# Performance work log

Measured on AMD Instinct MI355X. Metric: run time of the kernel, lower is better.

## Reference

```python
import jax, jax.numpy as jnp
import numpy as np

LOOP = 30  # kernel last-dim / loop count from original module

def setup_inputs() -> dict:
    key = jax.random.key(0)
    kB, k1, k2 = jax.random.split(key, 3)
    B = jax.random.normal(kB, (16, 64, 32, 32), dtype=jnp.float32)
    # torch.rand -> uniform [0,1)
    kernel1 = jax.random.uniform(k1, (64, 32, 32, LOOP), dtype=jnp.float32)
    kernel2 = jax.random.uniform(k2, (64, 32, 32, LOOP), dtype=jnp.float32)
    return {"B": B, "kernel1": kernel1, "kernel2": kernel2}

def reference(B, kernel1, kernel2):
    # fftshift over the 3 spatial dims, then the 30-iteration loop is batched:
    # move loop dim to front -> (30,64,32,32), broadcast against B (batch,64,32,32).
    Bs = jnp.fft.fftshift(B, axes=(-3, -2, -1))            # (batch,64,32,32)
    k1 = jnp.moveaxis(kernel1, -1, 0)                      # (30,64,32,32)
    k2 = jnp.moveaxis(kernel2, -1, 0)
    f1 = jnp.fft.fftn(Bs[:, None] * k1, axes=(-3, -2, -1))  # (batch,30,64,32,32) complex
    f2 = jnp.fft.fftn(Bs[:, None] * k2, axes=(-3, -2, -1))
    # complex multiply-accumulate over the loop dim
    return jnp.sum(f1 * f2, axis=1)                        # (batch,64,32,32) complex
```

## Files before the change

kernel.cpp:

```cpp
#include <hip/hip_runtime.h>
#include <hip/hip_fp16.h>
#include <cstdint>
#include <cstddef>


__host__ __device__ constexpr float twc(int k) {
  switch (k & 31) {
    case 0: return 1.0f;        case 1: return 0.98078528f;
    case 2: return 0.92387953f; case 3: return 0.83146961f;
    case 4: return 0.70710678f; case 5: return 0.55557023f;
    case 6: return 0.38268343f; case 7: return 0.19509032f;
    case 8: return 0.0f;        case 9: return -0.19509032f;
    case 10: return -0.38268343f; case 11: return -0.55557023f;
    case 12: return -0.70710678f; case 13: return -0.83146961f;
    case 14: return -0.92387953f; case 15: return -0.98078528f;
    default: return 0.0f;
  }
}
__host__ __device__ constexpr float tws(int k) {
  switch (k & 31) {
    case 0: return 0.0f;        case 1: return 0.19509032f;
    case 2: return 0.38268343f; case 3: return 0.55557023f;
    case 4: return 0.70710678f; case 5: return 0.83146961f;
    case 6: return 0.92387953f; case 7: return 0.98078528f;
    case 8: return 1.0f;        case 9: return 0.98078528f;
    case 10: return 0.92387953f; case 11: return 0.83146961f;
    case 12: return 0.70710678f; case 13: return 0.55557023f;
    case 14: return 0.38268343f; case 15: return 0.19509032f;
    default: return 0.0f;
  }
}

constexpr int brN(int x, int bits) {
  int r = 0;
  for (int b = 0; b < bits; ++b) { r = (r << 1) | (x & 1); x >>= 1; }
  return r;
}

template <int N>
__device__ __forceinline__ void fftN(float* xr, float* xi) {
#pragma unroll
  for (int len = 2; len <= N; len <<= 1) {
    const int half = len >> 1;
    const int step = 32 / len;
#pragma unroll
    for (int g = 0; g < N; g += len) {
#pragma unroll
      for (int j = 0; j < half; ++j) {
        const float c = twc(j * step), s = tws(j * step);
        const int lo = g + j, hi = g + j + half;
        float vr = xr[hi] * c + xi[hi] * s;
        float vi = xi[hi] * c - xr[hi] * s;
        float ur = xr[lo], ui = xi[lo];
        xr[lo] = ur + vr; xi[lo] = ui + vi;
        xr[hi] = ur - vr; xi[hi] = ui - vi;
      }
    }
  }
}

__global__ __launch_bounds__(256) void kzero(float4* __restrict__ o, int n4) {
  int i = blockIdx.x * 256 + threadIdx.x;
  if (i < n4) o[i] = make_float4(0.f, 0.f, 0.f, 0.f);
}


__global__ __launch_bounds__(256) void kpack(const float* __restrict__ k1,
                                             const float* __restrict__ k2,
                                             float2* __restrict__ kc) {
  int d0 = blockIdx.x >> 5, d1 = blockIdx.x & 31;
  __shared__ float2 s[960];
  int base = (d0 * 32 + d1) * 960;
  for (int u = threadIdx.x; u < 960; u += 256)
    s[u] = make_float2(k1[base + u], k2[base + u]);
  __syncthreads();
  for (int w = threadIdx.x; w < 960; w += 256) {
    int i = w >> 5, d2 = w & 31;
    kc[((size_t)(i * 64 + d0) * 32 + d1) * 32 + d2] = s[d2 * 30 + i];
  }
}

__global__ __launch_bounds__(256) void kfft2d_ws(const float* __restrict__ B,
                                                 const float2* __restrict__ kc,
                                                 __half2* __restrict__ Z,
                                                 int j0) {
  __shared__ float Lr[4][32 * 33];
  __shared__ float Li[4][32 * 33];

  const int t = threadIdx.x;
  const int v = blockIdx.x >> 4;
  const int q4 = blockIdx.x & 15;
  const int job = j0 + v;
  const int b = job / 30;
  const int i = job - b * 30;

  const int g = t >> 6;
  const int bc = t & 31;
  const int hh = (t >> 5) & 1;
  const int fs = t >> 5;
  const int fr = t & 31;

  const float* Bb = B + ((size_t)b << 16);

  {
    const int n0 = (q4 << 2) | g;
    const int sn0 = (n0 + 32) & 63;
    const float* bp = Bb + (sn0 << 10);
    const int sc = (bc + 16) & 31;
    const float2* kcl = kc + (((size_t)i << 6 | n0) << 10);
#pragma unroll
    for (int vv = 0; vv < 16; ++vv) {
      const int n1 = (hh << 4) | vv;
      float bv = bp[(((n1 + 16) & 31) << 5) | sc];
      float2 kv = kcl[(n1 << 5) | bc];
      Lr[g][n1 * 33 + bc] = bv * kv.x;
      Li[g][n1 * 33 + bc] = bv * kv.y;
    }
  }
  __syncthreads();

  if (t < 128) {
    float xr[32], xi[32];
#pragma unroll
    for (int u = 0; u < 32; ++u) {
      int p = fr * 33 + brN(u, 5);
      xr[u] = Lr[fs][p]; xi[u] = Li[fs][p];
    }
    fftN<32>(xr, xi);
#pragma unroll
    for (int u = 0; u < 32; ++u) {
      int p = fr * 33 + u;
      Lr[fs][p] = xr[u]; Li[fs][p] = xi[u];
    }
  }
  __syncthreads();

  if (t < 128) {
    float xr[32], xi[32];
#pragma unroll
    for (int u = 0; u < 32; ++u) {
      int p = brN(u, 5) * 33 + fr;
      xr[u] = Lr[fs][p]; xi[u] = Li[fs][p];
    }
    fftN<32>(xr, xi);
#pragma unroll
    for (int u = 0; u < 32; ++u) {
      int p = u * 33 + fr;
      Lr[fs][p] = xr[u]; Li[fs][p] = xi[u];
    }
  }
  __syncthreads();

#pragma unroll
  for (int j = 0; j < 16; ++j) {
    int w = (j << 8) | t;
    int g2 = w >> 10, row = (w >> 5) & 31, col = w & 31;
    int d0w = (q4 << 2) | g2;
    Z[((size_t)(v * 32 + row) << 6 | d0w) << 5 | col] = __float22half2_rn(
        make_float2(Lr[g2][row * 33 + col], Li[g2][row * 33 + col]));
  }
}

__global__ __launch_bounds__(256) void kacc64(const __half2* __restrict__ Z,
                                              float* __restrict__ tmp,
                                              int b0, int cb) {
  __shared__ float Ar[64 * 33], Ai[64 * 33];
  __shared__ float Br[64 * 33], Bi[64 * 33];
  __shared__ float W64c[64], W64s[64];

  const int t = threadIdx.x;
  const int d1 = blockIdx.x & 31;
  const int r = blockIdx.x >> 5;
  const int bl = r % cb;
  const int ig = r / cb;
  const int b = b0 + bl;
  const int i0g = ig * 8;
  const int i1g = (i0g + 8) < 30 ? (i0g + 8) : 30;

  if (t < 64) {
    float sv, cv;
    __sincosf(6.283185307179586f / 64.0f * (float)t, &sv, &cv);
    W64c[t] = cv; W64s[t] = sv;
  }
  __syncthreads();

  const int qc = t >> 5;
  const int d2 = t & 31;

  float acc[8];
#pragma unroll
  for (int a = 0; a < 8; ++a) acc[a] = 0.f;

  for (int i = i0g; i < i1g; ++i) {
    const int v = bl * 30 + i;
    const __half2* zp = Z + ((size_t)(v * 32 + d1) << 11);
#pragma unroll
    for (int j = 0; j < 8; ++j) {
      int f = (j << 8) | t;
      float2 w = __half22float2(zp[f]);
      Ar[(f >> 5) * 33 + (f & 31)] = w.x;
      Ai[(f >> 5) * 33 + (f & 31)] = w.y;
    }
    __syncthreads();

    {
      float xr[8], xi[8];
#pragma unroll
      for (int u = 0; u < 8; ++u) {
        int n0 = qc + (brN(u, 3) << 3);
        xr[u] = Ar[n0 * 33 + d2]; xi[u] = Ai[n0 * 33 + d2];
      }
      fftN<8>(xr, xi);
#pragma unroll
      for (int c = 0; c < 8; ++c) {
        int m = (qc * c) & 63;
        float wc = W64c[m], ws = W64s[m];
        float hr = xr[c] * wc + xi[c] * ws;
        float hi = xi[c] * wc - xr[c] * ws;
        int q2 = (c << 3) | qc;
        Br[q2 * 33 + d2] = hr; Bi[q2 * 33 + d2] = hi;
      }
    }
    __syncthreads();

    {
      float xr[8], xi[8];
#pragma unroll
      for (int u = 0; u < 8; ++u) {
        int q2 = (qc << 3) | brN(u, 3);
        xr[u] = Br[q2 * 33 + d2]; xi[u] = Bi[q2 * 33 + d2];
      }
      fftN<8>(xr, xi);
#pragma unroll
      for (int a = 0; a < 8; ++a)
        acc[a] += 2.0f * xr[a] * xi[a];
    }
    __syncthreads();
  }

#pragma unroll
  for (int a = 0; a < 8; ++a) {
    int d0f = qc + (a << 3);
    size_t off = ((size_t)(b << 6 | d0f) << 10) | (d1 << 5) | d2;
    atomicAdd(&tmp[off], 0.25f * acc[a]);
  }
}

__global__ __launch_bounds__(256) void ksym(const float* __restrict__ tmp,
                                            float* __restrict__ out,
                                            int out_size) {
  int idx = blockIdx.x * 256 + threadIdx.x;
  if (idx >= out_size || idx >= 16 * 65536) return;
  int d2 = idx & 31, d1 = (idx >> 5) & 31, d0 = (idx >> 10) & 63, b = idx >> 16;
  int n = (b << 16) | (((64 - d0) & 63) << 10) | (((32 - d1) & 31) << 5) |
          ((32 - d2) & 31);
  out[idx] = tmp[idx] + tmp[n];
}

__global__ __launch_bounds__(256) void kfused(const float* __restrict__ B,
                                              const float* __restrict__ k1,
                                              const float* __restrict__ k2,
                                              float* __restrict__ out,
                                              int out_size) {
  __shared__ float Lr[4][32 * 33];
  __shared__ float Li[4][32 * 33];
  __shared__ float W64c[64], W64s[64];

  const int t = threadIdx.x;
  const int bid = blockIdx.x;
  const int b = bid & 15;
  const int iq = (bid >> 4) & 3;
  const int ns = bid >> 6;
  const int i0 = iq * 8;
  const int ni = (iq == 3) ? 6 : 8;
  const int k0base = ns * 8;

  if (t < 64) {
    float sv, cv;
    __sincosf(6.283185307179586f / 64.0f * (float)t, &sv, &cv);
    W64c[t] = cv; W64s[t] = sv;
  }
  __syncthreads();

  const int g = t >> 6;
  const int bc = t & 31;
  const int hh = (t >> 5) & 1;
  const int fs = t >> 5;
  const int fr = t & 31;
  const int w1 = t >> 5;
  const int w2 = t & 31;

  const float* Bb = B + ((size_t)b << 16);

  float Sig[8][4];
#pragma unroll
  for (int kg = 0; kg < 8; ++kg)
#pragma unroll
    for (int q = 0; q < 4; ++q) Sig[kg][q] = 0.f;

  for (int ii = 0; ii < ni; ++ii) {
    const int i = i0 + ii;

    float Zr[8][4], Zi[8][4];
#pragma unroll
    for (int kg = 0; kg < 8; ++kg)
#pragma unroll
      for (int q = 0; q < 4; ++q) { Zr[kg][q] = 0.f; Zi[kg][q] = 0.f; }

    for (int it = 0; it < 16; ++it) {
      const int n0 = (it << 2) | g;
      {
        const int sn0 = (n0 + 32) & 63;
        const float* bp = Bb + (sn0 << 10);
        const int sc = (bc + 16) & 31;
#pragma unroll
        for (int v = 0; v < 16; ++v) {
          const int n1 = (hh << 4) | v;
          float bv = bp[(((n1 + 16) & 31) << 5) | sc];
          int ke = (((n0 << 10) | (n1 << 5) | bc) * 30) + i;
          Lr[g][n1 * 33 + bc] = bv * k1[ke];
          Li[g][n1 * 33 + bc] = bv * k2[ke];
        }
      }
      __syncthreads();

      if (t < 128) {
        float xr[32], xi[32];
#pragma unroll
        for (int u = 0; u < 32; ++u) {
          int p = fr * 33 + brN(u, 5);
          xr[u] = Lr[fs][p]; xi[u] = Li[fs][p];
        }
        fftN<32>(xr, xi);
#pragma unroll
        for (int u = 0; u < 32; ++u) {
          int p = fr * 33 + u;
          Lr[fs][p] = xr[u]; Li[fs][p] = xi[u];
        }
      }
      __syncthreads();

      if (t < 128) {
        float xr[32], xi[32];
#pragma unroll
        for (int u = 0; u < 32; ++u) {
          int p = brN(u, 5) * 33 + fr;
          xr[u] = Lr[fs][p]; xi[u] = Li[fs][p];
        }
        fftN<32>(xr, xi);
#pragma unroll
        for (int u = 0; u < 32; ++u) {
          int p = u * 33 + fr;
          Lr[fs][p] = xr[u]; Li[fs][p] = xi[u];
        }
      }
      __syncthreads();

#pragma unroll 1
      for (int s = 0; s < 4; ++s) {
        const int n0s = (it << 2) | s;
        const int dm = n0s & 63;
        float yr[4], yi[4];
#pragma unroll
        for (int q = 0; q < 4; ++q) {
          int p = (w1 + (q << 3)) * 33 + w2;
          yr[q] = Lr[s][p]; yi[q] = Li[s][p];
        }
        int m = (k0base * n0s) & 63;
#pragma unroll
        for (int kg = 0; kg < 8; ++kg) {
          float c = W64c[m], sn = W64s[m];
#pragma unroll
          for (int q = 0; q < 4; ++q) {
            Zr[kg][q] += yr[q] * c + yi[q] * sn;
            Zi[kg][q] += yi[q] * c - yr[q] * sn;
          }
          m = (m + dm) & 63;
        }
      }
      __syncthreads();
    }

#pragma unroll
    for (int kg = 0; kg < 8; ++kg)
#pragma unroll
      for (int q = 0; q < 4; ++q)
        Sig[kg][q] += 2.0f * Zr[kg][q] * Zi[kg][q];
  }

#pragma unroll
  for (int kg = 0; kg < 8; ++kg) {
    const int k0 = k0base + kg;
    const int nk0 = (64 - k0) & 63;
#pragma unroll
    for (int q = 0; q < 4; ++q) {
      const int r1 = w1 + (q << 3);
      const float v = Sig[kg][q] * 0.25f;
      const int nr1 = (32 - r1) & 31;
      const int nw2 = (32 - w2) & 31;
      int off = (((b << 6) | k0) << 10) | (r1 << 5) | w2;
      int noff = (((b << 6) | nk0) << 10) | (nr1 << 5) | nw2;
      if (off < out_size) atomicAdd(&out[off], v);
      if (noff < out_size) atomicAdd(&out[noff], v);
    }
  }
}

extern "C" void kernel_launch(void* const* d_in, const int* in_sizes, int n_in,
                              void* d_out, int out_size, void* d_ws,
                              size_t ws_size, hipStream_t stream) {
  const float* B = (const float*)d_in[0];
  const float* k1 = (const float*)d_in[1];
  const float* k2 = (const float*)d_in[2];
  (void)in_sizes; (void)n_in;

  const size_t tmpB = 4ull << 20;
  const size_t Z1 = 30ull * 65536 * 4;
  const size_t kcB = 30ull * 65536 * 8;

  int nbcap = 0;
  if (ws_size >= tmpB + kcB + Z1)
    nbcap = (int)((ws_size - tmpB - kcB) / Z1);

  if (nbcap >= 1) {
    char* ws = (char*)d_ws;
    float* tmp = (float*)ws;
    float2* kc = (float2*)(ws + tmpB);
    __half2* Z = (__half2*)(ws + tmpB + kcB);
    int nb = nbcap > 16 ? 16 : nbcap;

    kzero<<<(out_size / 4 + 255) / 256, 256, 0, stream>>>((float4*)tmp,
                                                          out_size / 4);
    kpack<<<2048, 256, 0, stream>>>(k1, k2, kc);

    for (int b0 = 0; b0 < 16; b0 += nb) {
      int cb = (16 - b0) < nb ? (16 - b0) : nb;
      int j0 = b0 * 30;
      kfft2d_ws<<<cb * 30 * 16, 256, 0, stream>>>(B, kc, Z, j0);
      kacc64<<<cb * 32 * 4, 256, 0, stream>>>(Z, tmp, b0, cb);
    }

    ksym<<<(out_size + 255) / 256, 256, 0, stream>>>(tmp, (float*)d_out,
                                                     out_size);
  } else {
    int n4 = out_size >> 2;
    int zb = (n4 + 255) >> 8;
    if (zb > 0) kzero<<<zb, 256, 0, stream>>>((float4*)d_out, n4);
    kfused<<<512, 256, 0, stream>>>(B, k1, k2, (float*)d_out, out_size);
  }
}
```

Baseline: 124.7 us.

## Process eight 2D slices per block with XOR-swizzled shared memory

The 2D FFT kernel now gives each block 8 depth slices instead of 4, so all 256 threads run the row and column FFTs rather than only half of them. The padded 33-stride shared layout is replaced by a 32-stride layout with an XOR swizzle to avoid bank conflicts. The grid is halved to match. Shared memory per block doubles to 64KB, which may lower occupancy, and every thread now holds 64 floats of FFT state, which raises register pressure.

```diff
diff --git a/kernel.cpp b/kernel.cpp
--- a/kernel.cpp
+++ b/kernel.cpp
@@ -84,80 +84,78 @@
                                                  const float2* __restrict__ kc,
                                                  __half2* __restrict__ Z,
                                                  int j0) {
-  __shared__ float Lr[4][32 * 33];
-  __shared__ float Li[4][32 * 33];
+  __shared__ float Lr[8][1024];
+  __shared__ float Li[8][1024];
 
   const int t = threadIdx.x;
-  const int v = blockIdx.x >> 4;
-  const int q4 = blockIdx.x & 15;
+  const int v = blockIdx.x >> 3;
+  const int q3 = blockIdx.x & 7;
   const int job = j0 + v;
   const int b = job / 30;
   const int i = job - b * 30;
 
-  const int g = t >> 6;
-  const int bc = t & 31;
-  const int hh = (t >> 5) & 1;
-  const int fs = t >> 5;
-  const int fr = t & 31;
+  const int s = t >> 5;
+  const int lc = t & 31;
 
   const float* Bb = B + ((size_t)b << 16);
 
   {
-    const int n0 = (q4 << 2) | g;
+    const int n0 = (q3 << 3) | s;
     const int sn0 = (n0 + 32) & 63;
     const float* bp = Bb + (sn0 << 10);
-    const int sc = (bc + 16) & 31;
+    const int sc = (lc + 16) & 31;
     const float2* kcl = kc + (((size_t)i << 6 | n0) << 10);
-#pragma unroll
-    for (int vv = 0; vv < 16; ++vv) {
-      const int n1 = (hh << 4) | vv;
+#pragma unroll 8
+    for (int n1 = 0; n1 < 32; ++n1) {
       float bv = bp[(((n1 + 16) & 31) << 5) | sc];
-      float2 kv = kcl[(n1 << 5) | bc];
-      Lr[g][n1 * 33 + bc] = bv * kv.x;
-      Li[g][n1 * 33 + bc] = bv * kv.y;
-    }
-  }
-  __syncthreads();
-
-  if (t < 128) {
+      float2 kv = kcl[(n1 << 5) | lc];
+      const int p = (n1 << 5) | ((lc ^ n1) & 31);
+      Lr[s][p] = bv * kv.x;
+      Li[s][p] = bv * kv.y;
+    }
+  }
+  __syncthreads();
+
+  {
     float xr[32], xi[32];
 #pragma unroll
     for (int u = 0; u < 32; ++u) {
-      int p = fr * 33 + brN(u, 5);
-      xr[u] = Lr[fs][p]; xi[u] = Li[fs][p];
+      int p = (lc << 5) | ((brN(u, 5) ^ lc) & 31);
+      xr[u] = Lr[s][p]; xi[u] = Li[s][p];
     }
     fftN<32>(xr, xi);
 #pragma unroll
     for (int u = 0; u < 32; ++u) {
-      int p = fr * 33 + u;
-      Lr[fs][p] = xr[u]; Li[fs][p] = xi[u];
-    }
-  }
-  __syncthreads();
-
-  if (t < 128) {
+      int p = (lc << 5) | ((u ^ lc) & 31);
+      Lr[s][p] = xr[u]; Li[s][p] = xi[u];
+    }
+  }
+  __syncthreads();
+
+  {
     float xr[32], xi[32];
 #pragma unroll
     for (int u = 0; u < 32; ++u) {
-      int p = brN(u, 5) * 33 + fr;
-      xr[u] = Lr[fs][p]; xi[u] = Li[fs][p];
+      int row = brN(u, 5);
+      int p = (row << 5) | ((lc ^ row) & 31);
+      xr[u] = Lr[s][p]; xi[u] = Li[s][p];
     }
     fftN<32>(xr, xi);
 #pragma unroll
     for (int u = 0; u < 32; ++u) {
-      int p = u * 33 + fr;
-      Lr[fs][p] = xr[u]; Li[fs][p] = xi[u];
-    }
-  }
-  __syncthreads();
-
-#pragma unroll
-  for (int j = 0; j < 16; ++j) {
-    int w = (j << 8) | t;
-    int g2 = w >> 10, row = (w >> 5) & 31, col = w & 31;
-    int d0w = (q4 << 2) | g2;
-    Z[((size_t)(v * 32 + row) << 6 | d0w) << 5 | col] = __float22half2_rn(
-        make_float2(Lr[g2][row * 33 + col], Li[g2][row * 33 + col]));
+      int p = (u << 5) | ((lc ^ u) & 31);
+      Lr[s][p] = xr[u]; Li[s][p] = xi[u];
+    }
+  }
+  __syncthreads();
+
+#pragma unroll 4
+  for (int j = 0; j < 32; ++j) {
+    int u = (j << 8) | t;
+    int col = u & 31, sl = (u >> 5) & 7, row = u >> 8;
+    int p = (row << 5) | ((col ^ row) & 31);
+    Z[((size_t)(v * 32 + row) << 6 | ((q3 << 3) | sl)) << 5 | col] =
+        __float22half2_rn(make_float2(Lr[sl][p], Li[sl][p]));
   }
 }
 
@@ -357,14 +355,14 @@
       __syncthreads();
 
 #pragma unroll 1
-      for (int s = 0; s < 4; ++s) {
-        const int n0s = (it << 2) | s;
+      for (int sq = 0; sq < 4; ++sq) {
+        const int n0s = (it << 2) | sq;
         const int dm = n0s & 63;
         float yr[4], yi[4];
 #pragma unroll
         for (int q = 0; q < 4; ++q) {
           int p = (w1 + (q << 3)) * 33 + w2;
-          yr[q] = Lr[s][p]; yi[q] = Li[s][p];
+          yr[q] = Lr[sq][p]; yi[q] = Li[sq][p];
         }
         int m = (k0base * n0s) & 63;
 #pragma unroll
@@ -436,7 +434,7 @@
     for (int b0 = 0; b0 < 16; b0 += nb) {
       int cb = (16 - b0) < nb ? (16 - b0) : nb;
       int j0 = b0 * 30;
-      kfft2d_ws<<<cb * 30 * 16, 256, 0, stream>>>(B, kc, Z, j0);
+      kfft2d_ws<<<cb * 30 * 8, 256, 0, stream>>>(B, kc, Z, j0);
       kacc64<<<cb * 32 * 4, 256, 0, stream>>>(Z, tmp, b0, cb);
     }
 
```

Measured after the change: 131.6 us. 1.06x slower.
